# Kernel optimization log

Measured on AMD Instinct MI355X. Metric: run time of the kernel, lower is better.

## Reference

```python
import jax, jax.numpy as jnp
import numpy as np

V, E, H, D, A, P = 8000, 384, 512, 512, 512, 128
B, N = 16, 128
NEG = -1.0e9


def _lstm(x, Wih, Whh, b, reverse=False):
    # x: (B, T, E); torch gate order i, f, g, o
    Hd = Whh.shape[1]
    def step(carry, xt):
        h, c = carry
        gates = xt @ Wih.T + h @ Whh.T + b
        i, f, g, o = jnp.split(gates, 4, axis=-1)
        c = jax.nn.sigmoid(f) * c + jax.nn.sigmoid(i) * jnp.tanh(g)
        h = jax.nn.sigmoid(o) * jnp.tanh(c)
        return (h, c), h
    xs = jnp.swapaxes(x, 0, 1)
    if reverse:
        xs = xs[::-1]
    init = (jnp.zeros((x.shape[0], Hd), x.dtype), jnp.zeros((x.shape[0], Hd), x.dtype))
    _, hs = jax.lax.scan(step, init, xs)
    if reverse:
        hs = hs[::-1]
    return jnp.swapaxes(hs, 0, 1)


def _forward(src_ids, src_mask, confusionset_mask, emb, Wih_f, Whh_f, b_f, Wih_b, Whh_b, b_b,
             Wih_d, Whh_d, b_d, W1, W2, v_att, combine_W, combine_b, vocab_W, vocab_b,
             Wg_W, Wg_b, ptr_W, ptr_b, ps_W, ps_b):
    x = emb[src_ids]                                                     # (B,N,E)
    # bidirectional encoder
    enc_hs = jnp.concatenate([_lstm(x, Wih_f, Whh_f, b_f),
                              _lstm(x, Wih_b, Whh_b, b_b, reverse=True)], axis=-1)  # (B,N,2H)
    # decoder LSTMCell unrolled over max_len=N steps (teacher forcing on src chars)
    dec_h = _lstm(x, Wih_d, Whh_d, b_d)                                  # (B,N,D)
    # Bahdanau additive attention
    dterm = dec_h @ W1.T                                                 # (B,N,A)
    eterm = enc_hs @ W2.T                                                # (B,N,A)
    score = jnp.tanh(dterm[:, :, None, :] + eterm[:, None, :, :]) @ v_att  # (B,T,n)
    score = jnp.where(src_mask[:, None, :] == 0, NEG, score)
    alpha = jax.nn.softmax(score, axis=-1)
    context = jnp.einsum('btn,bnh->bth', alpha, enc_hs)                  # (B,T,2H)
    combined = jnp.tanh(jnp.concatenate([dec_h, context], axis=-1) @ combine_W.T + combine_b)  # (B,T,D)
    vocab_logits = combined @ vocab_W.T + vocab_b                        # (B,T,V)
    vocab_logits = jnp.where(confusionset_mask == 0, NEG, vocab_logits)
    # pointer logits: Locj = (t == j) indicator as extra feature
    loc = jnp.eye(N, dtype=combined.dtype)                               # (T,n)
    base = combined @ ptr_W[:, :D].T + ptr_b                             # (B,T,P)
    ph = jnp.tanh(base[:, :, None, :] + loc[None, :, :, None] * ptr_W[:, D][None, None, None, :])  # (B,T,n,P)
    pos_scores = ph @ ps_W + ps_b                                        # (B,T,n)
    sentinel = jnp.tanh(combined @ Wg_W.T + Wg_b).sum(-1, keepdims=True) # (B,T,1)
    pointer_logits = jnp.concatenate([pos_scores, sentinel], axis=-1)    # (B,T,n+1)
    pad_mask = jnp.concatenate([src_mask, jnp.ones((src_mask.shape[0], 1), src_mask.dtype)], axis=1)
    pointer_logits = jnp.where(pad_mask[:, None, :] == 0, NEG, pointer_logits)
    return pointer_logits, vocab_logits


def setup_inputs():
    ks = iter(jax.random.split(jax.random.key(0), 40))
    def g(shape, s=0.05):
        return jax.random.normal(next(ks), shape, jnp.float32) * s
    inp = {
        'src_ids': jax.random.randint(next(ks), (B, N), 1, V),
        'src_mask': jnp.ones((B, N), jnp.int32),
        'confusionset_mask': jax.random.randint(next(ks), (B, N, V), 0, 2).astype(jnp.int32),
        'emb': g((V, E)).at[0].set(0.0),  # padding_idx=0 row zeroed
        'Wih_f': g((4 * H, E)), 'Whh_f': g((4 * H, H)), 'b_f': g((4 * H,)),
        'Wih_b': g((4 * H, E)), 'Whh_b': g((4 * H, H)), 'b_b': g((4 * H,)),
        'Wih_d': g((4 * D, E)), 'Whh_d': g((4 * D, D)), 'b_d': g((4 * D,)),
        'W1': g((A, D)), 'W2': g((A, 2 * H)), 'v_att': g((A,)),
        'combine_W': g((D, D + 2 * H)), 'combine_b': g((D,)),
        'vocab_W': g((V, D)), 'vocab_b': g((V,)),
        'Wg_W': g((D, D)), 'Wg_b': g((D,)),
        'ptr_W': g((P, D + 1)), 'ptr_b': g((P,)),
        'ps_W': g((P,)), 'ps_b': g(()),
    }
    return inp


def reference(src_ids, src_mask, confusionset_mask, emb, Wih_f, Whh_f, b_f, Wih_b, Whh_b, b_b,
              Wih_d, Whh_d, b_d, W1, W2, v_att, combine_W, combine_b, vocab_W, vocab_b,
              Wg_W, Wg_b, ptr_W, ptr_b, ps_W, ps_b):
    return _forward(src_ids, src_mask, confusionset_mask, emb, Wih_f, Whh_f, b_f, Wih_b, Whh_b, b_b,
                    Wih_d, Whh_d, b_d, W1, W2, v_att, combine_W, combine_b, vocab_W, vocab_b,
                    Wg_W, Wg_b, ptr_W, ptr_b, ps_W, ps_b)
```

## Files before the change

### kernel.cpp

```cpp
#include <hip/hip_runtime.h>
#include <hip/hip_bf16.h>
#include <math.h>

#define NEGV -1000000000.0f

static constexpr int B_ = 16, N_ = 128, BN_ = 2048;
static constexpr int E_ = 384, V_ = 8000;

typedef __attribute__((ext_vector_type(8))) short short8v;
typedef __attribute__((ext_vector_type(4))) float f32x4;

__device__ inline float wave_sum(float v) {
#pragma unroll
  for (int o = 32; o; o >>= 1) v += __shfl_xor(v, o);
  return v;
}
__device__ inline float wave_max(float v) {
#pragma unroll
  for (int o = 32; o; o >>= 1) v = fmaxf(v, __shfl_xor(v, o));
  return v;
}
__device__ inline float fast_tanh(float x) {
  return 1.f - 2.f / (1.f + __expf(2.f * x));
}
__device__ inline float fast_sig(float x) {
  return 1.f / (1.f + __expf(-x));
}
__device__ __forceinline__ void gl16(const void* g, void* l) {
  __builtin_amdgcn_global_load_lds((const __attribute__((address_space(1))) void*)g,
                                   (__attribute__((address_space(3))) void*)l, 16, 0, 0);
}

__global__ __launch_bounds__(256) void embed_kernel(
    const int* __restrict__ ids, const float* __restrict__ emb,
    __hip_bfloat16* __restrict__ xb) {
  const int row = blockIdx.x;
  const int id = ids[row];
  for (int e = threadIdx.x; e < E_; e += 256)
    xb[(size_t)row * E_ + e] = __float2bfloat16(emb[(size_t)id * E_ + e]);
}

struct CastArgs {
  const float* s[12];
  unsigned long long d[12];
  int base[12];
  int total;
};
__global__ __launch_bounds__(256) void cast_kernel(CastArgs a) {
  const int nq = a.total >> 2;
  for (int q = blockIdx.x * 256 + threadIdx.x; q < nq; q += gridDim.x * 256) {
    const int e = q << 2;
    int k = 11;
    while (e < a.base[k]) --k;
    const int i = e - a.base[k];
    __hip_bfloat16* dst = (__hip_bfloat16*)a.d[k] + i;
    if (k == 11) {
      const int row = i >> 9, col = i & 511;
      const float* sp = a.s[k] + (size_t)row * 513 + col;
#pragma unroll
      for (int u = 0; u < 4; ++u) dst[u] = __float2bfloat16(sp[u]);
    } else {
      float4 v = *(const float4*)(a.s[k] + i);
      __hip_bfloat16 h0 = __float2bfloat16(v.x), h1 = __float2bfloat16(v.y);
      __hip_bfloat16 h2 = __float2bfloat16(v.z), h3 = __float2bfloat16(v.w);
      ushort4 u4 = {*(unsigned short*)&h0, *(unsigned short*)&h1,
                    *(unsigned short*)&h2, *(unsigned short*)&h3};
      *(ushort4*)dst = u4;
    }
  }
}

template <int ACT, bool MASK, int TROUT>
__global__ __launch_bounds__(256) void bgemm_kernel(
    const __hip_bfloat16* __restrict__ A, int lda,
    const __hip_bfloat16* __restrict__ W, int ldw,
    const float* __restrict__ bias,
    float* __restrict__ C, int ldc,
    __hip_bfloat16* __restrict__ Cb, int ldcb,
    int M, int N, int K,
    const int* __restrict__ mask, int ldm,
    long aBs, long wBs, long cBs) {
  __shared__ __hip_bfloat16 Al[2][4096];
  __shared__ __hip_bfloat16 Bl[2][4096];
  A += (size_t)blockIdx.z * aBs;
  W += (size_t)blockIdx.z * wBs;
  const int tid = threadIdx.x;
  const int wid = tid >> 6, lane = tid & 63;
  const int m0 = blockIdx.y * 128, n0 = blockIdx.x * 128;
  const int nkt = K >> 5;
  const int rm = (wid >> 1) << 6, rn = (wid & 1) << 6;
  const int lrow = lane & 15, kq = lane >> 4;
  const int fs = ((lrow >> 1) & 3) << 4;

  f32x4 acc[4][4];
#pragma unroll
  for (int i = 0; i < 4; ++i)
#pragma unroll
    for (int j = 0; j < 4; ++j) acc[i][j] = {0.f, 0.f, 0.f, 0.f};

  auto stage = [&](int bi, int kt) {
#pragma unroll
    for (int c = 0; c < 2; ++c) {
      const int p = ((c * 4 + wid) << 6) + lane;
      const int row = p >> 2, cb = (p & 3) << 4;
      const int sw = ((row >> 1) & 3) << 4;
      const unsigned loff = (unsigned)__builtin_amdgcn_readfirstlane((c * 4 + wid) << 10);
      {
        const char* src = (const char*)A + ((size_t)(m0 + row) * lda + (size_t)kt * 32) * 2 + (cb ^ sw);
        gl16(src, (char*)&Al[bi][0] + loff);
      }
      {
        int gr = n0 + row;
        if (gr >= N) gr = N - 1;
        const char* src = (const char*)W + ((size_t)gr * ldw + (size_t)kt * 32) * 2 + (cb ^ sw);
        gl16(src, (char*)&Bl[bi][0] + loff);
      }
    }
  };
  auto compute = [&](int bi) {
    const char* Ab = (const char*)&Al[bi][0];
    const char* Bb = (const char*)&Bl[bi][0];
    const int roff = (kq << 4) ^ fs;
    short8v a[4], b[4];
#pragma unroll
    for (int i = 0; i < 4; ++i)
      a[i] = *(const short8v*)(Ab + (rm + i * 16 + lrow) * 64 + roff);
#pragma unroll
    for (int j = 0; j < 4; ++j)
      b[j] = *(const short8v*)(Bb + (rn + j * 16 + lrow) * 64 + roff);
#pragma unroll
    for (int i = 0; i < 4; ++i)
#pragma unroll
      for (int j = 0; j < 4; ++j)
        acc[i][j] = __builtin_amdgcn_mfma_f32_16x16x32_bf16(a[i], b[j], acc[i][j], 0, 0, 0);
  };

  stage(0, 0);
  for (int kt = 0; kt < nkt; ++kt) {
    __syncthreads();
    if (kt + 1 < nkt) stage((kt + 1) & 1, kt + 1);
    compute(kt & 1);
  }

#pragma unroll
  for (int i = 0; i < 4; ++i) {
#pragma unroll
    for (int r = 0; r < 4; ++r) {
      const int m = m0 + rm + i * 16 + kq * 4 + r;
#pragma unroll
      for (int j = 0; j < 4; ++j) {
        const int n = n0 + rn + j * 16 + lrow;
        if (n < N) {
          float v = acc[i][j][r] + (bias ? bias[n] : 0.f);
          if (ACT == 1) v = tanhf(v);
          if (MASK) {
            if (mask[(size_t)m * ldm + n] == 0) v = NEGV;
          }
          if (TROUT == 1) {
            Cb[(((size_t)(m >> 7) * 512 + n) << 7) + (m & 127)] = __float2bfloat16(v);
          } else {
            if (C) C[(size_t)m * ldc + n] = v;
            if (Cb) Cb[(size_t)m * ldcb + n + (size_t)blockIdx.z * cBs] = __float2bfloat16(v);
          }
        }
      }
    }
  }
}

__global__ __launch_bounds__(256) void lstm_kernel(
    const __hip_bfloat16* __restrict__ xp16,
    const __hip_bfloat16* __restrict__ whh16,
    __hip_bfloat16* __restrict__ hbuf) {
  const int l = blockIdx.x >> 5, g = blockIdx.x & 31;
  const int tid = threadIdx.x, lane = tid & 63, wid = tid >> 6;
  extern __shared__ char sm[];
  char* smW = sm;
  char* smH = sm + 65536;
  __hip_bfloat16* hout = (__hip_bfloat16*)(sm + 65536 + 16384);

  const __hip_bfloat16* wsrc = whh16 + (size_t)l * 2048 * 512;
  for (int p = tid; p < 4096; p += 256) {
    const int r = p >> 6, cb = (p & 63) << 4;
    const int grow = (r & 3) * 512 + (g << 4) + (r >> 2);
    float4 v = *(const float4*)((const char*)(wsrc + (size_t)grow * 512) + cb);
    *(float4*)(smW + r * 1024 + (cb ^ ((r & 7) << 4))) = v;
  }

  const int lrow = lane & 15, kq = lane >> 4;
  const int swz = (lrow & 7) << 4;
  const char* aB = smW + (wid * 16 + lrow) * 1024;
  const char* bB = smH + lrow * 1024;
  const int dl16 = wid * 4 + kq;
  const int dg = (g << 4) + dl16;
  const int bb = lrow;
  const bool rev = (l == 1);
  const __hip_bfloat16* xl = xp16 + (size_t)l * 2048 * 2048;
  __hip_bfloat16* hb_l = hbuf + (size_t)l * 128 * 8192;
  const int gq = tid >> 3;
  const int b0 = (tid & 7) * 2;
  const int gb = gq * 32;
  const int sw0 = (b0 & 7) << 4, sw1 = ((b0 + 1) & 7) << 4;
  float c = 0.f;

  for (int s = 0; s < 128; ++s) {
    const int t = rev ? 127 - s : s;
    const size_t xro = (size_t)(bb * 128 + t) * 2048 + dg;
    const float xgi = __bfloat162float(xl[xro]);
    const float xgf = __bfloat162float(xl[xro + 512]);
    const float xgg = __bfloat162float(xl[xro + 1024]);
    const float xgo = __bfloat162float(xl[xro + 1536]);

    if (s > 0) {
      if (gq != g) {
        const char* hsrc = (const char*)(hb_l + (size_t)(s - 1) * 8192);
        const unsigned loff = (unsigned)(tid * 64);
        unsigned hv;
        while (true) {
          asm volatile(
              "global_load_ushort %0, %1, %2 sc0 sc1\n\t"
              "s_waitcnt vmcnt(0)"
              : "=&v"(hv) : "v"(loff), "s"(hsrc) : "memory");
          if ((hv & 0xffffu) != 0x7f7fu) break;
          __builtin_amdgcn_s_sleep(1);
        }
        f32x4 q0, q1, q2, q3;
        asm volatile(
            "global_load_dwordx4 %0, %4, %5 sc0 sc1\n\t"
            "global_load_dwordx4 %1, %4, %5 offset:16 sc0 sc1\n\t"
            "global_load_dwordx4 %2, %4, %5 offset:32 sc0 sc1\n\t"
            "global_load_dwordx4 %3, %4, %5 offset:48 sc0 sc1\n\t"
            "s_waitcnt vmcnt(0)"
            : "=&v"(q0), "=&v"(q1), "=&v"(q2), "=&v"(q3)
            : "v"(loff), "s"(hsrc) : "memory");
        *(f32x4*)(smH + b0 * 1024 + (gb ^ sw0)) = q0;
        *(f32x4*)(smH + b0 * 1024 + ((gb + 16) ^ sw0)) = q1;
        *(f32x4*)(smH + (b0 + 1) * 1024 + (gb ^ sw1)) = q2;
        *(f32x4*)(smH + (b0 + 1) * 1024 + ((gb + 16) ^ sw1)) = q3;
      }
    } else {
      const f32x4 z = {0.f, 0.f, 0.f, 0.f};
      *(f32x4*)(smH + b0 * 1024 + (gb ^ sw0)) = z;
      *(f32x4*)(smH + b0 * 1024 + ((gb + 16) ^ sw0)) = z;
      *(f32x4*)(smH + (b0 + 1) * 1024 + (gb ^ sw1)) = z;
      *(f32x4*)(smH + (b0 + 1) * 1024 + ((gb + 16) ^ sw1)) = z;
    }
    __syncthreads();

    f32x4 acc0 = {0.f, 0.f, 0.f, 0.f}, acc1 = {0.f, 0.f, 0.f, 0.f};
#pragma unroll
    for (int kt = 0; kt < 16; kt += 2) {
      const int off0 = ((kt * 64 + (kq << 4)) ^ swz);
      const int off1 = (((kt + 1) * 64 + (kq << 4)) ^ swz);
      short8v a0 = *(const short8v*)(aB + off0);
      short8v b0v = *(const short8v*)(bB + off0);
      short8v a1 = *(const short8v*)(aB + off1);
      short8v b1v = *(const short8v*)(bB + off1);
      acc0 = __builtin_amdgcn_mfma_f32_16x16x32_bf16(a0, b0v, acc0, 0, 0, 0);
      acc1 = __builtin_amdgcn_mfma_f32_16x16x32_bf16(a1, b1v, acc1, 0, 0, 0);
    }
    const f32x4 acc = acc0 + acc1;
    __syncthreads();

    const float gi = acc[0] + xgi;
    const float gf = acc[1] + xgf;
    const float gg = acc[2] + xgg;
    const float go = acc[3] + xgo;
    c = fmaf(fast_sig(gf), c, fast_sig(gi) * fast_tanh(gg));
    const float h = fast_sig(go) * fast_tanh(c);
    __hip_bfloat16 hb16 = __float2bfloat16(h);
    const unsigned short hraw = *(unsigned short*)&hb16;
    hout[bb * 16 + dl16] = hb16;
    *(unsigned short*)(smH + bb * 1024 +
                       ((((g << 4) + dl16) * 2) ^ ((bb & 7) << 4))) = hraw;
    __syncthreads();
    if (tid < 32) {
      f32x4 hv4 = *(const f32x4*)((const char*)hout + tid * 16);
      char* hdst = (char*)(hb_l + (size_t)s * 8192);
      asm volatile("global_store_dwordx4 %0, %1, %2 sc0 sc1"
                   :: "v"((unsigned)((g << 9) + tid * 16)), "v"(hv4), "s"(hdst)
                   : "memory");
    }
  }
}

__global__ __launch_bounds__(256) void scatter_kernel(
    const __hip_bfloat16* __restrict__ hbuf,
    __hip_bfloat16* __restrict__ ehsb, __hip_bfloat16* __restrict__ ehsT,
    __hip_bfloat16* __restrict__ catb) {
  const int bid = blockIdx.x;
  const int l = bid >> 7, b = (bid >> 3) & 15, dgrp = bid & 7;
  const int tid = threadIdx.x;
  __shared__ unsigned short tile[64][130];
  const int t4 = tid >> 6, dl = tid & 63;
  const bool rev = (l == 1);
  const char* hb = (const char*)(hbuf + (size_t)l * 128 * 8192);
  for (int tt = 0; tt < 128; tt += 4) {
    const int t = tt + t4;
    const int s = rev ? 127 - t : t;
    const unsigned off = (unsigned)(s * 16384 + (dgrp * 4 + (dl >> 4)) * 512 +
                                    b * 32 + (dl & 15) * 2);
    unsigned hv;
    asm volatile("global_load_ushort %0, %1, %2 sc0 sc1\n\ts_waitcnt vmcnt(0)"
                 : "=&v"(hv) : "v"(off), "s"(hb) : "memory");
    tile[dl][t] = (unsigned short)hv;
  }
  __syncthreads();
  if (l < 2) {
    const int r = tid >> 2, seg = tid & 3;
    ushort4* dstT = (ushort4*)(ehsT + ((size_t)b * 1024 + l * 512 + dgrp * 64 + r) * 128 + seg * 32);
    const unsigned short* srcT = &tile[r][seg * 32];
#pragma unroll
    for (int q = 0; q < 8; ++q) dstT[q] = *(const ushort4*)(srcT + q * 4);
    const int t2 = tid >> 1, half = tid & 1;
    unsigned short buf[32];
#pragma unroll
    for (int q = 0; q < 32; ++q) buf[q] = tile[half * 32 + q][t2];
    ushort4* dstB = (ushort4*)(ehsb + ((size_t)(b * 128 + t2)) * 1024 + l * 512 + dgrp * 64 + half * 32);
#pragma unroll
    for (int q = 0; q < 8; ++q) dstB[q] = *(const ushort4*)(buf + q * 4);
  } else {
    const int t2 = tid >> 1, half = tid & 1;
    unsigned short buf[32];
#pragma unroll
    for (int q = 0; q < 32; ++q) buf[q] = tile[half * 32 + q][t2];
    ushort4* dstB = (ushort4*)(catb + ((size_t)(b * 128 + t2)) * 1536 + dgrp * 64 + half * 32);
#pragma unroll
    for (int q = 0; q < 8; ++q) dstB[q] = *(const ushort4*)(buf + q * 4);
  }
}

__global__ __launch_bounds__(256) void score_kernel(
    const float* __restrict__ dterm, const __hip_bfloat16* __restrict__ etT,
    const float* __restrict__ v_att, const int* __restrict__ src_mask,
    __hip_bfloat16* __restrict__ alphab) {
  const int bt = blockIdx.x, b = bt >> 7;
  const int tid = threadIdx.x;
  __shared__ float dt[512], vs[512], red[4][128], al[128], rtmp[2];
  dt[tid] = dterm[(size_t)bt * 512 + tid];
  dt[tid + 256] = dterm[(size_t)bt * 512 + 256 + tid];
  vs[tid] = v_att[tid];
  vs[tid + 256] = v_att[256 + tid];
  __syncthreads();
  const int n0 = (tid & 63) << 1, ah = tid >> 6;
  {
    const __hip_bfloat16* ep = etT + (((size_t)b * 512 + ah * 128) << 7) + n0;
    const float* dp = dt + ah * 128;
    const float* vp = vs + ah * 128;
    float p0 = 0.f, p1 = 0.f;
    for (int a = 0; a < 128; ++a) {
      const unsigned u = *(const unsigned*)(ep + ((size_t)a << 7));
      unsigned u0 = u << 16, u1 = u & 0xffff0000u;
      const float e0 = *(float*)&u0, e1 = *(float*)&u1;
      const float da = dp[a], va = vp[a];
      p0 = fmaf(va, fast_tanh(da + e0), p0);
      p1 = fmaf(va, fast_tanh(da + e1), p1);
    }
    red[ah][n0] = p0;
    red[ah][n0 + 1] = p1;
  }
  __syncthreads();
  if (tid < 128) {
    float s = red[0][tid] + red[1][tid] + red[2][tid] + red[3][tid];
    if (src_mask[b * 128 + tid] == 0) s = NEGV;
    al[tid] = s;
  }
  __syncthreads();
  if (tid < 64) {
    float m = fmaxf(al[tid], al[tid + 64]);
    m = wave_max(m);
    if (tid == 0) rtmp[0] = m;
  }
  __syncthreads();
  if (tid < 128) al[tid] = __expf(al[tid] - rtmp[0]);
  __syncthreads();
  if (tid < 64) {
    float s2 = al[tid] + al[tid + 64];
    s2 = wave_sum(s2);
    if (tid == 0) rtmp[1] = 1.f / s2;
  }
  __syncthreads();
  if (tid < 128)
    alphab[(size_t)bt * 128 + tid] = __float2bfloat16(al[tid] * rtmp[1]);
}

__global__ __launch_bounds__(256) void pointer_kernel(
    const float* __restrict__ base, const float* __restrict__ wgout,
    const float* __restrict__ ptr_W, const float* __restrict__ ps_W,
    const float* __restrict__ ps_b, const int* __restrict__ src_mask,
    float* __restrict__ out0) {
  const int bt = blockIdx.x;
  const int b = bt >> 7, t = bt & 127;
  const int tid = threadIdx.x;
  __shared__ float r0[4], r1[4], r2[4], fin[3];
  float off_p = 0.f, diag_p = 0.f, sent_p;
  if (tid < 128) {
    const float ba = base[(size_t)bt * 128 + tid];
    const float pw = ps_W[tid];
    off_p = tanhf(ba) * pw;
    diag_p = tanhf(ba + ptr_W[tid * 513 + 512]) * pw;
  }
  sent_p = wgout[(size_t)bt * 512 + tid] + wgout[(size_t)bt * 512 + 256 + tid];
  off_p = wave_sum(off_p);
  diag_p = wave_sum(diag_p);
  sent_p = wave_sum(sent_p);
  const int wid = tid >> 6, lane = tid & 63;
  if (lane == 0) { r0[wid] = off_p; r1[wid] = diag_p; r2[wid] = sent_p; }
  __syncthreads();
  if (tid == 0) {
    const float psb = ps_b[0];
    fin[0] = r0[0] + r0[1] + r0[2] + r0[3] + psb;
    fin[1] = r1[0] + r1[1] + r1[2] + r1[3] + psb;
    fin[2] = r2[0] + r2[1] + r2[2] + r2[3];
  }
  __syncthreads();
  const float s_off = fin[0], s_diag = fin[1], sent = fin[2];
  if (tid < 129) {
    float v;
    if (tid == 128) v = sent;
    else {
      v = (tid == t) ? s_diag : s_off;
      if (src_mask[b * 128 + tid] == 0) v = NEGV;
    }
    out0[(size_t)bt * 129 + tid] = v;
  }
}

extern "C" void kernel_launch(void* const* d_in, const int* in_sizes, int n_in,
                              void* d_out, int out_size, void* d_ws, size_t ws_size,
                              hipStream_t stream) {
  const int* src_ids   = (const int*)d_in[0];
  const int* src_mask  = (const int*)d_in[1];
  const int* cmask     = (const int*)d_in[2];
  const float* emb     = (const float*)d_in[3];
  const float* Wih_f   = (const float*)d_in[4];
  const float* Whh_f   = (const float*)d_in[5];
  const float* b_f     = (const float*)d_in[6];
  const float* Wih_b   = (const float*)d_in[7];
  const float* Whh_b   = (const float*)d_in[8];
  const float* b_b     = (const float*)d_in[9];
  const float* Wih_d   = (const float*)d_in[10];
  const float* Whh_d   = (const float*)d_in[11];
  const float* b_d     = (const float*)d_in[12];
  const float* W1      = (const float*)d_in[13];
  const float* W2      = (const float*)d_in[14];
  const float* v_att   = (const float*)d_in[15];
  const float* comb_W  = (const float*)d_in[16];
  const float* comb_b  = (const float*)d_in[17];
  const float* vocab_W = (const float*)d_in[18];
  const float* vocab_b = (const float*)d_in[19];
  const float* Wg_W    = (const float*)d_in[20];
  const float* Wg_b    = (const float*)d_in[21];
  const float* ptr_W   = (const float*)d_in[22];
  const float* ptr_b   = (const float*)d_in[23];
  const float* ps_W    = (const float*)d_in[24];
  const float* ps_b    = (const float*)d_in[25];
  (void)in_sizes; (void)n_in; (void)out_size; (void)ws_size;

  char* wsb = (char*)d_ws;
  size_t o = 0;
  auto alloc = [&](size_t bytes) { char* p = wsb + o; o = (o + bytes + 255) & ~(size_t)255; return p; };
  __hip_bfloat16* xb      = (__hip_bfloat16*)alloc((size_t)BN_ * E_ * 2);
  __hip_bfloat16* xproj16 = (__hip_bfloat16*)alloc((size_t)3 * BN_ * 2048 * 2);
  __hip_bfloat16* ehsb    = (__hip_bfloat16*)alloc((size_t)BN_ * 1024 * 2);
  __hip_bfloat16* ehsT    = (__hip_bfloat16*)alloc((size_t)16 * 1024 * 128 * 2);
  __hip_bfloat16* catb    = (__hip_bfloat16*)alloc((size_t)BN_ * 1536 * 2);
  float* dterm            = (float*)alloc((size_t)BN_ * 512 * 4);
  __hip_bfloat16* etT     = (__hip_bfloat16*)alloc((size_t)16 * 512 * 128 * 2);
  __hip_bfloat16* alphab  = (__hip_bfloat16*)alloc((size_t)BN_ * 128 * 2);
  __hip_bfloat16* combb   = (__hip_bfloat16*)alloc((size_t)BN_ * 512 * 2);
  float* wgout            = (float*)alloc((size_t)BN_ * 512 * 4);
  float* baseb            = (float*)alloc((size_t)BN_ * 128 * 4);
  __hip_bfloat16* hbuf    = (__hip_bfloat16*)alloc((size_t)3 * 128 * 8192 * 2);
  __hip_bfloat16* wihf16  = (__hip_bfloat16*)alloc((size_t)2048 * 384 * 2);
  __hip_bfloat16* wihb16  = (__hip_bfloat16*)alloc((size_t)2048 * 384 * 2);
  __hip_bfloat16* wihd16  = (__hip_bfloat16*)alloc((size_t)2048 * 384 * 2);
  __hip_bfloat16* whh16   = (__hip_bfloat16*)alloc((size_t)3 * 2048 * 512 * 2);
  __hip_bfloat16* w1_16   = (__hip_bfloat16*)alloc((size_t)512 * 512 * 2);
  __hip_bfloat16* w2_16   = (__hip_bfloat16*)alloc((size_t)512 * 1024 * 2);
  __hip_bfloat16* combw16 = (__hip_bfloat16*)alloc((size_t)512 * 1536 * 2);
  __hip_bfloat16* vocw16  = (__hip_bfloat16*)alloc((size_t)8000 * 512 * 2);
  __hip_bfloat16* wgw16   = (__hip_bfloat16*)alloc((size_t)512 * 512 * 2);
  __hip_bfloat16* ptrw16  = (__hip_bfloat16*)alloc((size_t)128 * 512 * 2);

  float* out0 = (float*)d_out;
  float* out1 = out0 + (size_t)BN_ * 129;

  hipError_t e0 = hipMemsetAsync(hbuf, 0x7f, (size_t)3 * 128 * 8192 * 2, stream);
  (void)e0;
  embed_kernel<<<BN_, 256, 0, stream>>>(src_ids, emb, xb);

  CastArgs ca;
  const float* srcs[12] = {Wih_f, Wih_b, Wih_d, Whh_f, Whh_b, Whh_d,
                           W1, W2, comb_W, vocab_W, Wg_W, ptr_W};
  __hip_bfloat16* dsts[12] = {wihf16, wihb16, wihd16, whh16, whh16 + 2048 * 512,
                              whh16 + 2 * 2048 * 512, w1_16, w2_16, combw16,
                              vocw16, wgw16, ptrw16};
  int ns[12] = {2048 * 384, 2048 * 384, 2048 * 384, 2048 * 512, 2048 * 512,
                2048 * 512, 512 * 512, 512 * 1024, 512 * 1536, 8000 * 512,
                512 * 512, 128 * 512};
  int acc = 0;
  for (int k = 0; k < 12; ++k) {
    ca.s[k] = srcs[k];
    ca.d[k] = (unsigned long long)dsts[k];
    ca.base[k] = acc;
    acc += ns[k];
  }
  ca.total = acc;
  cast_kernel<<<2048, 256, 0, stream>>>(ca);

  bgemm_kernel<0, false, 0><<<dim3(16, 16), 256, 0, stream>>>(
      xb, E_, wihf16, E_, b_f, nullptr, 0, xproj16, 2048, BN_, 2048, E_, nullptr, 0, 0, 0, 0);
  bgemm_kernel<0, false, 0><<<dim3(16, 16), 256, 0, stream>>>(
      xb, E_, wihb16, E_, b_b, nullptr, 0, xproj16 + (size_t)BN_ * 2048, 2048, BN_, 2048, E_, nullptr, 0, 0, 0, 0);
  bgemm_kernel<0, false, 0><<<dim3(16, 16), 256, 0, stream>>>(
      xb, E_, wihd16, E_, b_d, nullptr, 0, xproj16 + (size_t)2 * BN_ * 2048, 2048, BN_, 2048, E_, nullptr, 0, 0, 0, 0);

  hipError_t e1 = hipFuncSetAttribute((const void*)lstm_kernel,
                      hipFuncAttributeMaxDynamicSharedMemorySize, 82432);
  (void)e1;
  lstm_kernel<<<96, 256, 82432, stream>>>(xproj16, whh16, hbuf);

  scatter_kernel<<<384, 256, 0, stream>>>(hbuf, ehsb, ehsT, catb);

  bgemm_kernel<0, false, 0><<<dim3(4, 16), 256, 0, stream>>>(
      catb, 1536, w1_16, 512, nullptr, dterm, 512, nullptr, 0, BN_, 512, 512, nullptr, 0, 0, 0, 0);
  bgemm_kernel<0, false, 1><<<dim3(4, 16), 256, 0, stream>>>(
      ehsb, 1024, w2_16, 1024, nullptr, nullptr, 0, etT, 0, BN_, 512, 1024, nullptr, 0, 0, 0, 0);

  score_kernel<<<BN_, 256, 0, stream>>>(dterm, etT, v_att, src_mask, alphab);

  bgemm_kernel<0, false, 0><<<dim3(8, 1, 16), 256, 0, stream>>>(
      alphab, 128, ehsT, 128, nullptr, nullptr, 0, catb + 512, 1536,
      128, 1024, 128, nullptr, 0, 128 * 128, 1024 * 128, 128 * 1536);

  bgemm_kernel<1, false, 0><<<dim3(4, 16), 256, 0, stream>>>(
      catb, 1536, combw16, 1536, comb_b, nullptr, 0, combb, 512, BN_, 512, 1536, nullptr, 0, 0, 0, 0);

  bgemm_kernel<0, true, 0><<<dim3(63, 16), 256, 0, stream>>>(
      combb, 512, vocw16, 512, vocab_b, out1, V_, nullptr, 0, BN_, V_, 512, cmask, V_, 0, 0, 0);

  bgemm_kernel<1, false, 0><<<dim3(4, 16), 256, 0, stream>>>(
      combb, 512, wgw16, 512, Wg_b, wgout, 512, nullptr, 0, BN_, 512, 512, nullptr, 0, 0, 0, 0);

  bgemm_kernel<0, false, 0><<<dim3(1, 16), 256, 0, stream>>>(
      combb, 512, ptrw16, 512, ptr_b, baseb, 128, nullptr, 0, BN_, 128, 512, nullptr, 0, 0, 0, 0);

  pointer_kernel<<<BN_, 256, 0, stream>>>(baseb, wgout, ptr_W, ps_W, ps_b, src_mask, out0);
}
```

Before: 695.6 us.

## Add 64x64 GEMM variant, fuse Wg/ptr GEMMs, batch score rows, tighten LSTM polling

```diff
diff --git a/kernel.cpp b/kernel.cpp
--- a/kernel.cpp
+++ b/kernel.cpp
@@ -25,6 +25,18 @@
 }
 __device__ inline float fast_sig(float x) {
   return 1.f / (1.f + __expf(-x));
+}
+__device__ inline int ok16(const f32x4& f) {
+  const unsigned a = __builtin_bit_cast(unsigned, f[0]);
+  const unsigned b = __builtin_bit_cast(unsigned, f[1]);
+  const unsigned c = __builtin_bit_cast(unsigned, f[2]);
+  const unsigned d = __builtin_bit_cast(unsigned, f[3]);
+  int r = 1;
+  r &= ((a & 0xffffu) != 0x7f7fu) & ((a >> 16) != 0x7f7fu);
+  r &= ((b & 0xffffu) != 0x7f7fu) & ((b >> 16) != 0x7f7fu);
+  r &= ((c & 0xffffu) != 0x7f7fu) & ((c >> 16) != 0x7f7fu);
+  r &= ((d & 0xffffu) != 0x7f7fu) & ((d >> 16) != 0x7f7fu);
+  return r;
 }
 __device__ __forceinline__ void gl16(const void* g, void* l) {
   __builtin_amdgcn_global_load_lds((const __attribute__((address_space(1))) void*)g,
@@ -70,7 +82,7 @@
   }
 }
 
-template <int ACT, bool MASK, int TROUT>
+template <int ACT, bool MASK>
 __global__ __launch_bounds__(256) void bgemm_kernel(
     const __hip_bfloat16* __restrict__ A, int lda,
     const __hip_bfloat16* __restrict__ W, int ldw,
@@ -78,12 +90,9 @@
     float* __restrict__ C, int ldc,
     __hip_bfloat16* __restrict__ Cb, int ldcb,
     int M, int N, int K,
-    const int* __restrict__ mask, int ldm,
-    long aBs, long wBs, long cBs) {
+    const int* __restrict__ mask, int ldm) {
   __shared__ __hip_bfloat16 Al[2][4096];
   __shared__ __hip_bfloat16 Bl[2][4096];
-  A += (size_t)blockIdx.z * aBs;
-  W += (size_t)blockIdx.z * wBs;
   const int tid = threadIdx.x;
   const int wid = tid >> 6, lane = tid & 63;
   const int m0 = blockIdx.y * 128, n0 = blockIdx.x * 128;
@@ -156,6 +165,98 @@
           if (MASK) {
             if (mask[(size_t)m * ldm + n] == 0) v = NEGV;
           }
+          if (C) C[(size_t)m * ldc + n] = v;
+          if (Cb) Cb[(size_t)m * ldcb + n] = __float2bfloat16(v);
+        }
+      }
+    }
+  }
+}
+
+template <int ACT, int TROUT>
+__global__ __launch_bounds__(256) void bgemm64_kernel(
+    const __hip_bfloat16* __restrict__ A, int lda,
+    const __hip_bfloat16* __restrict__ W, int ldw,
+    const float* __restrict__ bias, const float* __restrict__ bias2,
+    float* __restrict__ C, int ldc, float* __restrict__ C2,
+    __hip_bfloat16* __restrict__ Cb, int ldcb,
+    int M, int N, int K,
+    long aBs, long wBs, long cBs) {
+  __shared__ __hip_bfloat16 Al[2][2048];
+  __shared__ __hip_bfloat16 Bl[2][2048];
+  A += (size_t)blockIdx.z * aBs;
+  W += (size_t)blockIdx.z * wBs;
+  const int tid = threadIdx.x;
+  const int wid = tid >> 6, lane = tid & 63;
+  const int m0 = blockIdx.y * 64, n0 = blockIdx.x * 64;
+  const int nkt = K >> 5;
+  const int rm = (wid >> 1) << 5, rn = (wid & 1) << 5;
+  const int lrow = lane & 15, kq = lane >> 4;
+  const int fs = ((lrow >> 1) & 3) << 4;
+
+  f32x4 acc[2][2];
+#pragma unroll
+  for (int i = 0; i < 2; ++i)
+#pragma unroll
+    for (int j = 0; j < 2; ++j) acc[i][j] = {0.f, 0.f, 0.f, 0.f};
+
+  auto stage = [&](int bi, int kt) {
+    const int p = tid;
+    const int row = p >> 2, cb = (p & 3) << 4;
+    const int sw = ((row >> 1) & 3) << 4;
+    const unsigned loff = (unsigned)__builtin_amdgcn_readfirstlane(wid << 10);
+    {
+      const char* src = (const char*)A + ((size_t)(m0 + row) * lda + (size_t)kt * 32) * 2 + (cb ^ sw);
+      gl16(src, (char*)&Al[bi][0] + loff);
+    }
+    {
+      const char* src = (const char*)W + ((size_t)(n0 + row) * ldw + (size_t)kt * 32) * 2 + (cb ^ sw);
+      gl16(src, (char*)&Bl[bi][0] + loff);
+    }
+  };
+  auto compute = [&](int bi) {
+    const char* Ab = (const char*)&Al[bi][0];
+    const char* Bb = (const char*)&Bl[bi][0];
+    const int roff = (kq << 4) ^ fs;
+    short8v a[2], b[2];
+#pragma unroll
+    for (int i = 0; i < 2; ++i)
+      a[i] = *(const short8v*)(Ab + (rm + i * 16 + lrow) * 64 + roff);
+#pragma unroll
+    for (int j = 0; j < 2; ++j)
+      b[j] = *(const short8v*)(Bb + (rn + j * 16 + lrow) * 64 + roff);
+#pragma unroll
+    for (int i = 0; i < 2; ++i)
+#pragma unroll
+      for (int j = 0; j < 2; ++j)
+        acc[i][j] = __builtin_amdgcn_mfma_f32_16x16x32_bf16(a[i], b[j], acc[i][j], 0, 0, 0);
+  };
+
+  stage(0, 0);
+  for (int kt = 0; kt < nkt; ++kt) {
+    __syncthreads();
+    if (kt + 1 < nkt) stage((kt + 1) & 1, kt + 1);
+    compute(kt & 1);
+  }
+
+#pragma unroll
+  for (int i = 0; i < 2; ++i) {
+#pragma unroll
+    for (int r = 0; r < 4; ++r) {
+      const int m = m0 + rm + i * 16 + kq * 4 + r;
+#pragma unroll
+      for (int j = 0; j < 2; ++j) {
+        const int n = n0 + rn + j * 16 + lrow;
+        float v = acc[i][j][r];
+        if (TROUT == 2) {
+          if (n < 512) {
+            C[(size_t)m * ldc + n] = tanhf(v + bias[n]);
+          } else {
+            C2[(size_t)m * 128 + (n - 512)] = v + bias2[n - 512];
+          }
+        } else {
+          v += (bias ? bias[n] : 0.f);
+          if (ACT == 1) v = tanhf(v);
           if (TROUT == 1) {
             Cb[(((size_t)(m >> 7) * 512 + n) << 7) + (m & 127)] = __float2bfloat16(v);
           } else {
@@ -215,24 +316,20 @@
       if (gq != g) {
         const char* hsrc = (const char*)(hb_l + (size_t)(s - 1) * 8192);
         const unsigned loff = (unsigned)(tid * 64);
-        unsigned hv;
+        f32x4 q0, q1, q2, q3;
         while (true) {
           asm volatile(
-              "global_load_ushort %0, %1, %2 sc0 sc1\n\t"
+              "global_load_dwordx4 %0, %4, %5 sc0 sc1\n\t"
+              "global_load_dwordx4 %1, %4, %5 offset:16 sc0 sc1\n\t"
+              "global_load_dwordx4 %2, %4, %5 offset:32 sc0 sc1\n\t"
+              "global_load_dwordx4 %3, %4, %5 offset:48 sc0 sc1\n\t"
               "s_waitcnt vmcnt(0)"
-              : "=&v"(hv) : "v"(loff), "s"(hsrc) : "memory");
-          if ((hv & 0xffffu) != 0x7f7fu) break;
+              : "=&v"(q0), "=&v"(q1), "=&v"(q2), "=&v"(q3)
+              : "v"(loff), "s"(hsrc)
+              : "memory");
+          if (ok16(q0) & ok16(q1) & ok16(q2) & ok16(q3)) break;
           __builtin_amdgcn_s_sleep(1);
         }
-        f32x4 q0, q1, q2, q3;
-        asm volatile(
-            "global_load_dwordx4 %0, %4, %5 sc0 sc1\n\t"
-            "global_load_dwordx4 %1, %4, %5 offset:16 sc0 sc1\n\t"
-            "global_load_dwordx4 %2, %4, %5 offset:32 sc0 sc1\n\t"
-            "global_load_dwordx4 %3, %4, %5 offset:48 sc0 sc1\n\t"
-            "s_waitcnt vmcnt(0)"
-            : "=&v"(q0), "=&v"(q1), "=&v"(q2), "=&v"(q3)
-            : "v"(loff), "s"(hsrc) : "memory");
         *(f32x4*)(smH + b0 * 1024 + (gb ^ sw0)) = q0;
         *(f32x4*)(smH + b0 * 1024 + ((gb + 16) ^ sw0)) = q1;
         *(f32x4*)(smH + (b0 + 1) * 1024 + (gb ^ sw1)) = q2;
@@ -260,7 +357,6 @@
       acc1 = __builtin_amdgcn_mfma_f32_16x16x32_bf16(a1, b1v, acc1, 0, 0, 0);
     }
     const f32x4 acc = acc0 + acc1;
-    __syncthreads();
 
     const float gi = acc[0] + xgi;
     const float gf = acc[1] + xgf;
@@ -271,9 +367,9 @@
     __hip_bfloat16 hb16 = __float2bfloat16(h);
     const unsigned short hraw = *(unsigned short*)&hb16;
     hout[bb * 16 + dl16] = hb16;
+    __syncthreads();
     *(unsigned short*)(smH + bb * 1024 +
                        ((((g << 4) + dl16) * 2) ^ ((bb & 7) << 4))) = hraw;
-    __syncthreads();
     if (tid < 32) {
       f32x4 hv4 = *(const f32x4*)((const char*)hout + tid * 16);
       char* hdst = (char*)(hb_l + (size_t)s * 8192);
@@ -295,15 +391,30 @@
   const int t4 = tid >> 6, dl = tid & 63;
   const bool rev = (l == 1);
   const char* hb = (const char*)(hbuf + (size_t)l * 128 * 8192);
-  for (int tt = 0; tt < 128; tt += 4) {
-    const int t = tt + t4;
-    const int s = rev ? 127 - t : t;
-    const unsigned off = (unsigned)(s * 16384 + (dgrp * 4 + (dl >> 4)) * 512 +
-                                    b * 32 + (dl & 15) * 2);
-    unsigned hv;
-    asm volatile("global_load_ushort %0, %1, %2 sc0 sc1\n\ts_waitcnt vmcnt(0)"
-                 : "=&v"(hv) : "v"(off), "s"(hb) : "memory");
-    tile[dl][t] = (unsigned short)hv;
+  const unsigned lineoff = (unsigned)((dgrp * 4 + (dl >> 4)) * 512 + b * 32 + (dl & 15) * 2);
+  for (int u = 0; u < 8; ++u) {
+    const int tbase = t4 * 4 + u * 16;
+    unsigned o[4];
+#pragma unroll
+    for (int w = 0; w < 4; ++w) {
+      const int t = tbase + w;
+      const int s = rev ? 127 - t : t;
+      o[w] = (unsigned)(s * 16384) + lineoff;
+    }
+    unsigned h0, h1, h2, h3;
+    asm volatile(
+        "global_load_ushort %0, %4, %8 sc0 sc1\n\t"
+        "global_load_ushort %1, %5, %8 sc0 sc1\n\t"
+        "global_load_ushort %2, %6, %8 sc0 sc1\n\t"
+        "global_load_ushort %3, %7, %8 sc0 sc1\n\t"
+        "s_waitcnt vmcnt(0)"
+        : "=&v"(h0), "=&v"(h1), "=&v"(h2), "=&v"(h3)
+        : "v"(o[0]), "v"(o[1]), "v"(o[2]), "v"(o[3]), "s"(hb)
+        : "memory");
+    tile[dl][tbase] = (unsigned short)h0;
+    tile[dl][tbase + 1] = (unsigned short)h1;
+    tile[dl][tbase + 2] = (unsigned short)h2;
+    tile[dl][tbase + 3] = (unsigned short)h3;
   }
   __syncthreads();
   if (l < 2) {
@@ -334,54 +445,64 @@
     const float* __restrict__ dterm, const __hip_bfloat16* __restrict__ etT,
     const float* __restrict__ v_att, const int* __restrict__ src_mask,
     __hip_bfloat16* __restrict__ alphab) {
-  const int bt = blockIdx.x, b = bt >> 7;
+  const int b = blockIdx.x >> 5, tg = blockIdx.x & 31;
+  const int t0 = tg * 4;
   const int tid = threadIdx.x;
-  __shared__ float dt[512], vs[512], red[4][128], al[128], rtmp[2];
-  dt[tid] = dterm[(size_t)bt * 512 + tid];
-  dt[tid + 256] = dterm[(size_t)bt * 512 + 256 + tid];
+  __shared__ float dt[4][512], vs[512], red[4][4][128], al[4][128];
+  for (int i = tid; i < 2048; i += 256)
+    dt[i >> 9][i & 511] = dterm[((size_t)(b * 128 + t0 + (i >> 9))) * 512 + (i & 511)];
   vs[tid] = v_att[tid];
   vs[tid + 256] = v_att[256 + tid];
   __syncthreads();
   const int n0 = (tid & 63) << 1, ah = tid >> 6;
   {
     const __hip_bfloat16* ep = etT + (((size_t)b * 512 + ah * 128) << 7) + n0;
-    const float* dp = dt + ah * 128;
     const float* vp = vs + ah * 128;
-    float p0 = 0.f, p1 = 0.f;
+    const float* dp0 = &dt[0][ah * 128];
+    const float* dp1 = &dt[1][ah * 128];
+    const float* dp2 = &dt[2][ah * 128];
+    const float* dp3 = &dt[3][ah * 128];
+    float p00 = 0, p01 = 0, p10 = 0, p11 = 0, p20 = 0, p21 = 0, p30 = 0, p31 = 0;
     for (int a = 0; a < 128; ++a) {
       const unsigned u = *(const unsigned*)(ep + ((size_t)a << 7));
       unsigned u0 = u << 16, u1 = u & 0xffff0000u;
-      const float e0 = *(float*)&u0, e1 = *(float*)&u1;
-      const float da = dp[a], va = vp[a];
-      p0 = fmaf(va, fast_tanh(da + e0), p0);
-      p1 = fmaf(va, fast_tanh(da + e1), p1);
-    }
-    red[ah][n0] = p0;
-    red[ah][n0 + 1] = p1;
+      const float e0 = __builtin_bit_cast(float, u0);
+      const float e1 = __builtin_bit_cast(float, u1);
+      const float va = vp[a];
+      p00 = fmaf(va, fast_tanh(dp0[a] + e0), p00);
+      p01 = fmaf(va, fast_tanh(dp0[a] + e1), p01);
+      p10 = fmaf(va, fast_tanh(dp1[a] + e0), p10);
+      p11 = fmaf(va, fast_tanh(dp1[a] + e1), p11);
+      p20 = fmaf(va, fast_tanh(dp2[a] + e0), p20);
+      p21 = fmaf(va, fast_tanh(dp2[a] + e1), p21);
+      p30 = fmaf(va, fast_tanh(dp3[a] + e0), p30);
+      p31 = fmaf(va, fast_tanh(dp3[a] + e1), p31);
+    }
+    red[0][ah][n0] = p00; red[0][ah][n0 + 1] = p01;
+    red[1][ah][n0] = p10; red[1][ah][n0 + 1] = p11;
+    red[2][ah][n0] = p20; red[2][ah][n0 + 1] = p21;
+    red[3][ah][n0] = p30; red[3][ah][n0 + 1] = p31;
   }
   __syncthreads();
-  if (tid < 128) {
-    float s = red[0][tid] + red[1][tid] + red[2][tid] + red[3][tid];
-    if (src_mask[b * 128 + tid] == 0) s = NEGV;
-    al[tid] = s;
+#pragma unroll
+  for (int tp = 0; tp < 2; ++tp) {
+    const int tt = tp * 2 + (tid >> 7);
+    const int n = tid & 127;
+    float sc = red[tt][0][n] + red[tt][1][n] + red[tt][2][n] + red[tt][3][n];
+    if (src_mask[b * 128 + n] == 0) sc = NEGV;
+    al[tt][n] = sc;
   }
   __syncthreads();
-  if (tid < 64) {
-    float m = fmaxf(al[tid], al[tid + 64]);
-    m = wave_max(m);
-    if (tid == 0) rtmp[0] = m;
-  }
-  __syncthreads();
-  if (tid < 128) al[tid] = __expf(al[tid] - rtmp[0]);
-  __syncthreads();
-  if (tid < 64) {
-    float s2 = al[tid] + al[tid + 64];
-    s2 = wave_sum(s2);
-    if (tid == 0) rtmp[1] = 1.f / s2;
-  }
-  __syncthreads();
-  if (tid < 128)
-    alphab[(size_t)bt * 128 + tid] = __float2bfloat16(al[tid] * rtmp[1]);
+  {
+    const int tt = tid >> 6, lane = tid & 63;
+    const float v0 = al[tt][lane], v1 = al[tt][lane + 64];
+    const float m = wave_max(fmaxf(v0, v1));
+    const float e0 = __expf(v0 - m), e1 = __expf(v1 - m);
+    const float inv = 1.f / wave_sum(e0 + e1);
+    __hip_bfloat16* ap = alphab + ((size_t)(b * 128 + t0 + tt)) * 128;
+    ap[lane] = __float2bfloat16(e0 * inv);
+    ap[lane + 64] = __float2bfloat16(e1 * inv);
+  }
 }
 
 __global__ __launch_bounds__(256) void pointer_kernel(
@@ -509,12 +630,12 @@
   ca.total = acc;
   cast_kernel<<<2048, 256, 0, stream>>>(ca);
 
-  bgemm_kernel<0, false, 0><<<dim3(16, 16), 256, 0, stream>>>(
-      xb, E_, wihf16, E_, b_f, nullptr, 0, xproj16, 2048, BN_, 2048, E_, nullptr, 0, 0, 0, 0);
-  bgemm_kernel<0, false, 0><<<dim3(16, 16), 256, 0, stream>>>(
-      xb, E_, wihb16, E_, b_b, nullptr, 0, xproj16 + (size_t)BN_ * 2048, 2048, BN_, 2048, E_, nullptr, 0, 0, 0, 0);
-  bgemm_kernel<0, false, 0><<<dim3(16, 16), 256, 0, stream>>>(
-      xb, E_, wihd16, E_, b_d, nullptr, 0, xproj16 + (size_t)2 * BN_ * 2048, 2048, BN_, 2048, E_, nullptr, 0, 0, 0, 0);
+  bgemm_kernel<0, false><<<dim3(16, 16), 256, 0, stream>>>(
+      xb, E_, wihf16, E_, b_f, nullptr, 0, xproj16, 2048, BN_, 2048, E_, nullptr, 0);
+  bgemm_kernel<0, false><<<dim3(16, 16), 256, 0, stream>>>(
+      xb, E_, wihb16, E_, b_b, nullptr, 0, xproj16 + (size_t)BN_ * 2048, 2048, BN_, 2048, E_, nullptr, 0);
+  bgemm_kernel<0, false><<<dim3(16, 16), 256, 0, stream>>>(
+      xb, E_, wihd16, E_, b_d, nullptr, 0, xproj16 + (size_t)2 * BN_ * 2048, 2048, BN_, 2048, E_, nullptr, 0);
 
   hipError_t e1 = hipFuncSetAttribute((const void*)lstm_kernel,
                       hipFuncAttributeMaxDynamicSharedMemorySize, 82432);
@@ -523,28 +644,29 @@
 
   scatter_kernel<<<384, 256, 0, stream>>>(hbuf, ehsb, ehsT, catb);
 
-  bgemm_kernel<0, false, 0><<<dim3(4, 16), 256, 0, stream>>>(
-      catb, 1536, w1_16, 512, nullptr, dterm, 512, nullptr, 0, BN_, 512, 512, nullptr, 0, 0, 0, 0);
-  bgemm_kernel<0, false, 1><<<dim3(4, 16), 256, 0, stream>>>(
-      ehsb, 1024, w2_16, 1024, nullptr, nullptr, 0, etT, 0, BN_, 512, 1024, nullptr, 0, 0, 0, 0);
-
-  score_kernel<<<BN_, 256, 0, stream>>>(dterm, etT, v_att, src_mask, alphab);
-
-  bgemm_kernel<0, false, 0><<<dim3(8, 1, 16), 256, 0, stream>>>(
-      alphab, 128, ehsT, 128, nullptr, nullptr, 0, catb + 512, 1536,
-      128, 1024, 128, nullptr, 0, 128 * 128, 1024 * 128, 128 * 1536);
-
-  bgemm_kernel<1, false, 0><<<dim3(4, 16), 256, 0, stream>>>(
-      catb, 1536, combw16, 1536, comb_b, nullptr, 0, combb, 512, BN_, 512, 1536, nullptr, 0, 0, 0, 0);
-
-  bgemm_kernel<0, true, 0><<<dim3(63, 16), 256, 0, stream>>>(
-      combb, 512, vocw16, 512, vocab_b, out1, V_, nullptr, 0, BN_, V_, 512, cmask, V_, 0, 0, 0);
-
-  bgemm_kernel<1, false, 0><<<dim3(4, 16), 256, 0, stream>>>(
-      combb, 512, wgw16, 512, Wg_b, wgout, 512, nullptr, 0, BN_, 512, 512, nullptr, 0, 0, 0, 0);
-
-  bgemm_kernel<0, false, 0><<<dim3(1, 16), 256, 0, stream>>>(
-      combb, 512, ptrw16, 512, ptr_b, baseb, 128, nullptr, 0, BN_, 128, 512, nullptr, 0, 0, 0, 0);
+  bgemm64_kernel<0, 0><<<dim3(8, 32), 256, 0, stream>>>(
+      catb, 1536, w1_16, 512, nullptr, nullptr, dterm, 512, nullptr, nullptr, 0,
+      BN_, 512, 512, 0, 0, 0);
+  bgemm64_kernel<0, 1><<<dim3(8, 32), 256, 0, stream>>>(
+      ehsb, 1024, w2_16, 1024, nullptr, nullptr, nullptr, 0, nullptr, etT, 0,
+      BN_, 512, 1024, 0, 0, 0);
+
+  score_kernel<<<16 * 32, 256, 0, stream>>>(dterm, etT, v_att, src_mask, alphab);
+
+  bgemm64_kernel<0, 0><<<dim3(16, 2, 16), 256, 0, stream>>>(
+      alphab, 128, ehsT, 128, nullptr, nullptr, nullptr, 0, nullptr,
+      catb + 512, 1536, 128, 1024, 128, 128 * 128, 1024 * 128, 128 * 1536);
+
+  bgemm64_kernel<1, 0><<<dim3(8, 32), 256, 0, stream>>>(
+      catb, 1536, combw16, 1536, comb_b, nullptr, nullptr, 0, nullptr,
+      combb, 512, BN_, 512, 1536, 0, 0, 0);
+
+  bgemm_kernel<0, true><<<dim3(63, 16), 256, 0, stream>>>(
+      combb, 512, vocw16, 512, vocab_b, out1, V_, nullptr, 0, BN_, V_, 512, cmask, V_);
+
+  bgemm64_kernel<0, 2><<<dim3(10, 32), 256, 0, stream>>>(
+      combb, 512, wgw16, 512, Wg_b, ptr_b, wgout, 512, baseb, nullptr, 0,
+      BN_, 640, 512, 0, 0, 0);
 
   pointer_kernel<<<BN_, 256, 0, stream>>>(baseb, wgout, ptr_W, ps_W, ps_b, src_mask, out0);
 }
```

Result: faster. 657.7 us (-5.5%).
